# Optimization experiments

Hardware: AMD Instinct MI355X
Metric: run time of the kernel (lower is better)

Reference implementation:

```python
import jax, jax.numpy as jnp
import numpy as np

B, T, D = 1, 2048, 4096
N, K, H = 32, 8, 128  # num_heads, num_kv_heads, head_dim
ROPE_BASE = 10000
SCALE_FACTOR = 1.0
EPS = 1e-6
NEG_INF = -1e9


def rms_norm(x):
    var = jnp.mean(jnp.square(x), axis=-1, keepdims=True)
    return x * jax.lax.rsqrt(var + EPS)


def apply_rope(x, positions, base_frequency, scale_factor=1.0):
    # x: [B, L, num_heads, H], positions: [B, L]
    head_dim = x.shape[-1]
    fraction = 2.0 * jnp.arange(head_dim // 2, dtype=jnp.float32) / head_dim
    timescale = base_frequency ** fraction  # [H/2]
    sinusoid = positions[..., None].astype(jnp.float32) / timescale  # [B,L,H/2]
    sinusoid = sinusoid[..., None, :] / scale_factor  # [B,L,1,H/2]
    sin, cos = jnp.sin(sinusoid), jnp.cos(sinusoid)
    x1, x2 = jnp.split(x, 2, axis=-1)
    return jnp.concatenate([x1 * cos - x2 * sin, x2 * cos + x1 * sin], axis=-1)


def setup_inputs() -> dict:
    key = jax.random.key(0)
    ks = jax.random.split(key, 7)
    x = jax.random.normal(ks[0], (B, T, D), dtype=jnp.float32)
    segment_pos = jnp.broadcast_to(jnp.arange(T, dtype=jnp.int32)[None, :], (B, T))
    causal = jnp.tril(jnp.ones((T, T), dtype=bool))
    attn_mask = jnp.where(causal, 0.0, NEG_INF).astype(jnp.float32)[None]  # [B,T,S]
    attn_mask = jnp.broadcast_to(attn_mask, (B, T, T))
    q_w = jax.random.normal(ks[1], (N, D, H), dtype=jnp.float32) * (D ** -0.5)
    kv_w = jax.random.normal(ks[2], (2, K, D, H), dtype=jnp.float32) * (D ** -0.5)
    o_w = jax.random.normal(ks[3], (N, H, D), dtype=jnp.float32) * ((N * H) ** -0.5)
    q_scale = jax.random.normal(ks[4], (H,), dtype=jnp.float32) * 0.02  # RMSNorm scale (zeros-init style)
    k_scale = jax.random.normal(ks[5], (H,), dtype=jnp.float32) * 0.02
    return {"x": x, "segment_pos": segment_pos, "attn_mask": attn_mask,
            "q_w": q_w, "kv_w": kv_w, "o_w": o_w,
            "q_scale": q_scale, "k_scale": k_scale}


def reference(x, segment_pos, attn_mask, q_w, kv_w, o_w, q_scale, k_scale):
    # Projections
    q = jnp.einsum('BTD,NDH->BTNH', x, q_w)          # [B,T,N,H]
    kv = jnp.einsum('BSD,CKDH->CBSKH', x, kv_w)      # [2,B,S,K,H]
    k, v = kv[0], kv[1]
    # QK RMSNorm (with scale, (1+scale) convention) and value RMSNorm (no scale)
    q = rms_norm(q) * (1.0 + q_scale)
    k = rms_norm(k) * (1.0 + k_scale)
    v = rms_norm(v)
    # RoPE (standard path: positions are [B,L])
    q = apply_rope(q, segment_pos, ROPE_BASE, SCALE_FACTOR)
    k = apply_rope(k, segment_pos, ROPE_BASE, SCALE_FACTOR)
    # GQA grouping: [B,T,K,G,H]
    G = N // K
    qg = q.reshape(B, T, K, G, H)
    attn_logits = jnp.einsum('btkgh,bskh->bkgts', qg, k)  # [B,K,G,T,S]
    attn_logits = attn_logits + attn_mask[:, None, None, :, :]
    attn_weights = jax.nn.softmax(attn_logits, axis=-1).astype(v.dtype)
    out = jnp.einsum('bkgts,bskh->btkgh', attn_weights, v)  # [B,T,K,G,H]
    out = out.reshape(B, T, N, H)
    return jnp.einsum('BTNH,NHD->BTD', out, o_w)
```

## Files before the change

kernel.cpp:

```cpp
#include <hip/hip_runtime.h>
#include <stdint.h>


typedef __bf16 bf16x8 __attribute__((ext_vector_type(8)));
typedef float  f32x4  __attribute__((ext_vector_type(4)));

__device__ __forceinline__ uint16_t f2bf(float f) {
    union { float f; uint32_t u; } v; v.f = f;
    uint32_t r = v.u + 0x7fffu + ((v.u >> 16) & 1u);
    return (uint16_t)(r >> 16);
}

__device__ __forceinline__ void gload_lds16(const void* g, void* l) {
    __builtin_amdgcn_global_load_lds(
        (const __attribute__((address_space(1))) uint32_t*)g,
        (__attribute__((address_space(3))) uint32_t*)l, 16, 0, 0);
}

__global__ __launch_bounds__(256) void k_cvt_x(const float* __restrict__ x,
                                               uint16_t* __restrict__ xb) {
    int i = (blockIdx.x * 256 + threadIdx.x) * 8;
    int r = i >> 12, k = i & 4095;
    float4 a = *(const float4*)(x + i);
    float4 b = *(const float4*)(x + i + 4);
    uint16_t tmp[8];
    tmp[0] = f2bf(a.x); tmp[1] = f2bf(a.y); tmp[2] = f2bf(a.z); tmp[3] = f2bf(a.w);
    tmp[4] = f2bf(b.x); tmp[5] = f2bf(b.y); tmp[6] = f2bf(b.z); tmp[7] = f2bf(b.w);
    int dst = r * 4096 + (k & ~63) + (((((k >> 3) & 7) ^ (r & 7))) << 3);
    *(uint4*)(xb + dst) = *(uint4*)tmp;
}

__global__ __launch_bounds__(256) void k_prep_wt(const float* __restrict__ qw,
                                                 const float* __restrict__ kvw,
                                                 uint16_t* __restrict__ Wt) {
    const int hx = blockIdx.x, dx = blockIdx.y, m = blockIdx.z;
    const float* src = (m < 32) ? (qw + (size_t)m * 524288)
                                : (kvw + (size_t)(m - 32) * 524288);
    __shared__ uint16_t tile[64][65];
    const int t = threadIdx.x, d0 = dx * 64, h0 = hx * 64;
#pragma unroll
    for (int i = 0; i < 16; ++i) {
        int idx = i * 256 + t, r = idx >> 6, c = idx & 63;
        tile[r][c] = f2bf(src[(size_t)(d0 + r) * 128 + h0 + c]);
    }
    __syncthreads();
#pragma unroll
    for (int it = 0; it < 2; ++it) {
        int slot = it * 256 + t, hr = slot >> 3, cl = slot & 7;
        int R = m * 128 + h0 + hr;
        uint16_t tmp[8];
#pragma unroll
        for (int e = 0; e < 8; ++e) tmp[e] = tile[cl * 8 + e][hr];
        *(uint4*)&Wt[(size_t)R * 4096 + d0 + ((cl ^ (R & 7)) << 3)] = *(uint4*)tmp;
    }
}

__global__ __launch_bounds__(256) void k_prep_ot(const float* __restrict__ ow,
                                                 uint16_t* __restrict__ Ot) {
    const int dx = blockIdx.x, hx = blockIdx.y, n = blockIdx.z;
    const float* src = ow + (size_t)n * 524288;
    __shared__ uint16_t tile[64][65];
    const int t = threadIdx.x, h0 = hx * 64, d0 = dx * 64;
#pragma unroll
    for (int i = 0; i < 16; ++i) {
        int idx = i * 256 + t, r = idx >> 6, c = idx & 63;
        tile[r][c] = f2bf(src[(size_t)(h0 + r) * 4096 + d0 + c]);
    }
    __syncthreads();
#pragma unroll
    for (int it = 0; it < 2; ++it) {
        int slot = it * 256 + t, dr = slot >> 3, cl = slot & 7;
        int R = d0 + dr;
        uint16_t tmp[8];
#pragma unroll
        for (int e = 0; e < 8; ++e) tmp[e] = tile[cl * 8 + e][dr];
        *(uint4*)&Ot[(size_t)R * 4096 + n * 128 + h0 + ((cl ^ (R & 7)) << 3)] = *(uint4*)tmp;
    }
}


#define PH_BAR do { asm volatile("" ::: "memory"); \
                    __builtin_amdgcn_s_barrier(); \
                    asm volatile("" ::: "memory"); } while (0)
#define WAIT_LGKM do { asm volatile("s_waitcnt lgkmcnt(0)" ::: "memory"); \
                       __builtin_amdgcn_sched_barrier(0); } while (0)
#define WAIT_VM(N) do { asm volatile("s_waitcnt vmcnt(" #N ")" ::: "memory"); \
                        __builtin_amdgcn_sched_barrier(0); } while (0)

__global__ __launch_bounds__(512, 2) void k_gemm_qkv(const uint16_t* __restrict__ A,
                                                     const uint16_t* __restrict__ Bt,
                                                     const int* __restrict__ pos,
                                                     const float* __restrict__ qs,
                                                     const float* __restrict__ ks,
                                                     uint16_t* __restrict__ Qg,
                                                     uint16_t* __restrict__ Kg,
                                                     uint16_t* __restrict__ Vg) {
    extern __shared__ __align__(16) char smem[];
    uint16_t* lds = (uint16_t*)smem;
    const int Kd = 4096;
    const int t = threadIdx.x, wid = t >> 6, lane = t & 63;
    const int l16 = lane & 15, quad = lane >> 4;
    const int wr = wid >> 2, wc = wid & 3;
    const int bx = blockIdx.x, bm0 = blockIdx.y * 256, bn0 = bx * 256;

    f32x4 acc[8][4];
    const f32x4 z4 = {0.f, 0.f, 0.f, 0.f};
#pragma unroll
    for (int i = 0; i < 8; ++i)
#pragma unroll
        for (int j = 0; j < 4; ++j) acc[i][j] = z4;

    const int r0 = wid * 16 + (lane >> 2), c4 = lane & 3;
    const int sw2 = (r0 >> 1) & 3, sw7 = r0 & 7;
    const int offK0 = (((c4 ^ sw2)) ^ sw7) * 8;
    const int offK1 = ((4 + (c4 ^ sw2)) ^ sw7) * 8;
    const uint16_t* pA0 = A + (size_t)(bm0 + r0) * Kd;
    const uint16_t* pA1 = pA0 + (size_t)128 * Kd;
    const uint16_t* pB0 = Bt + (size_t)(bn0 + r0) * Kd;
    const uint16_t* pB1 = pB0 + (size_t)128 * Kd;
    uint16_t* stA = lds + wid * 512;
    uint16_t* stB = lds + 32768 + wid * 512;

    const int sA = (l16 >> 1) & 3;
    const int rdA = (wr * 128 + l16) * 32 + ((quad ^ sA) << 3);
    const int rdB = 32768 + (wc * 64 + l16) * 32 + ((quad ^ sA) << 3);

    bf16x8 af[8], bf0, bf1;

#define STAGE_A(SLAB, OFF, TT) do { \
    gload_lds16(pA0 + (size_t)(TT) * 64 + (OFF), stA + (SLAB) * 8192); \
    gload_lds16(pA1 + (size_t)(TT) * 64 + (OFF), stA + (SLAB) * 8192 + 4096); } while (0)
#define STAGE_B(SLAB, OFF, TT) do { \
    gload_lds16(pB0 + (size_t)(TT) * 64 + (OFF), stB + (SLAB) * 8192); \
    gload_lds16(pB1 + (size_t)(TT) * 64 + (OFF), stB + (SLAB) * 8192 + 4096); } while (0)
#define LOAD_AF(SLAB) do { _Pragma("unroll") \
    for (int i_ = 0; i_ < 8; ++i_) \
        af[i_] = *(const bf16x8*)&lds[(SLAB) * 8192 + rdA + i_ * 512]; } while (0)
#define LOAD_BF(SLAB, CH) do { \
    bf0 = *(const bf16x8*)&lds[(SLAB) * 8192 + rdB + (CH) * 1024]; \
    bf1 = *(const bf16x8*)&lds[(SLAB) * 8192 + rdB + (CH) * 1024 + 512]; } while (0)
#define MFMA_PH(CH) do { __builtin_amdgcn_s_setprio(1); \
    _Pragma("unroll") for (int i_ = 0; i_ < 8; ++i_) { \
        acc[i_][2*(CH)]   = __builtin_amdgcn_mfma_f32_16x16x32_bf16(af[i_], bf0, acc[i_][2*(CH)],   0, 0, 0); \
        acc[i_][2*(CH)+1] = __builtin_amdgcn_mfma_f32_16x16x32_bf16(af[i_], bf1, acc[i_][2*(CH)+1], 0, 0, 0); } \
    __builtin_amdgcn_s_setprio(0); } while (0)

#define TILE(TT, BUF) do { \
     \
    LOAD_AF(2*(BUF)); LOAD_BF(2*(BUF), 0); \
    STAGE_A((((BUF)^1)*2+1), offK1, (TT)+1); \
    PH_BAR; WAIT_LGKM; MFMA_PH(0); PH_BAR; \
     \
    LOAD_BF(2*(BUF), 1); \
    WAIT_VM(6); \
    STAGE_B((((BUF)^1)*2+1), offK1, (TT)+1); \
    PH_BAR; WAIT_LGKM; MFMA_PH(1); PH_BAR; \
     \
    LOAD_AF(2*(BUF)+1); LOAD_BF(2*(BUF)+1, 0); \
    STAGE_A((BUF)*2, offK0, (TT)+2); \
    PH_BAR; WAIT_LGKM; MFMA_PH(0); PH_BAR; \
     \
    LOAD_BF(2*(BUF)+1, 1); \
    WAIT_VM(6); \
    STAGE_B((BUF)*2, offK0, (TT)+2); \
    PH_BAR; WAIT_LGKM; MFMA_PH(1); PH_BAR; \
} while (0)

    STAGE_A(0, offK0, 0); STAGE_B(0, offK0, 0);
    STAGE_A(1, offK1, 0); STAGE_B(1, offK1, 0);
    STAGE_A(2, offK0, 1); STAGE_B(2, offK0, 1);
    WAIT_VM(8);
    PH_BAR;

#pragma unroll 1
    for (int Ti = 0; Ti < 31; ++Ti) {
        TILE(2 * Ti, 0);
        TILE(2 * Ti + 1, 1);
    }

    STAGE_A(3, offK1, 63); STAGE_B(3, offK1, 63);
    WAIT_VM(0);
    PH_BAR;
#pragma unroll
    for (int T = 62; T < 64; ++T) {
        const int BUF = T & 1;
        LOAD_AF(2*BUF);   LOAD_BF(2*BUF, 0);   PH_BAR; WAIT_LGKM; MFMA_PH(0); PH_BAR;
        LOAD_BF(2*BUF, 1);                     PH_BAR; WAIT_LGKM; MFMA_PH(1); PH_BAR;
        LOAD_AF(2*BUF+1); LOAD_BF(2*BUF+1, 0); PH_BAR; WAIT_LGKM; MFMA_PH(0); PH_BAR;
        LOAD_BF(2*BUF+1, 1);                   PH_BAR; WAIT_LGKM; MFMA_PH(1); PH_BAR;
    }

#undef TILE
#undef MFMA_PH
#undef LOAD_BF
#undef LOAD_AF
#undef STAGE_B
#undef STAGE_A

    float* X   = (float*)smem;
    float* ssq = (float*)(smem + 133120);

#pragma unroll
    for (int i = 0; i < 8; ++i)
#pragma unroll
        for (int r = 0; r < 4; ++r) {
            float s = 0.f;
#pragma unroll
            for (int j = 0; j < 4; ++j) s += acc[i][j][r] * acc[i][j][r];
            s += __shfl_xor(s, 1); s += __shfl_xor(s, 2);
            s += __shfl_xor(s, 4); s += __shfl_xor(s, 8);
            if (l16 == 0)
                ssq[(wr * 128 + i * 16 + quad * 4 + r) * 4 + (wc >> 1) * 2 + (wc & 1)] = s;
        }
    __syncthreads();

    const int cat = (bx < 16) ? 0 : (bx < 20 ? 1 : 2);
    float s1 = 0.f, s2 = 0.f, invts = 0.f;
    if (cat < 2) {
        const float* sc = cat ? ks : qs;
        s1 = 1.0f + sc[lane];
        s2 = 1.0f + sc[lane + 64];
        invts = exp2f((float)lane * -0.20762050593046014f);
    }

#pragma unroll
    for (int pass = 0; pass < 2; ++pass) {
        if (wr == pass) {
#pragma unroll
            for (int i = 0; i < 8; ++i)
#pragma unroll
                for (int j = 0; j < 4; ++j)
#pragma unroll
                    for (int r = 0; r < 4; ++r)
                        X[(i * 16 + quad * 4 + r) * 260 + wc * 64 + j * 16 + l16] = acc[i][j][r];
        }
        __syncthreads();
        for (int rr = 0; rr < 16; ++rr) {
            const int lrow = wid * 16 + rr;
            const int grow = bm0 + pass * 128 + lrow;
            float sn = 0.f, cs = 0.f;
            if (cat < 2) {
                float ang = (float)pos[grow] * invts;
                __sincosf(ang, &sn, &cs);
            }
#pragma unroll
            for (int hh = 0; hh < 2; ++hh) {
                const int sb = (pass * 128 + lrow) * 4 + hh * 2;
                float rn = rsqrtf((ssq[sb] + ssq[sb + 1]) * 0.0078125f + 1e-6f);
                float x1 = X[lrow * 260 + hh * 128 + lane];
                float x2 = X[lrow * 260 + hh * 128 + 64 + lane];
                if (cat < 2) {
                    float y1 = x1 * rn * s1, y2 = x2 * rn * s2;
                    X[lrow * 260 + hh * 128 + lane]      = y1 * cs - y2 * sn;
                    X[lrow * 260 + hh * 128 + 64 + lane] = y2 * cs + y1 * sn;
                } else {
                    X[lrow * 260 + hh * 128 + lane]      = x1 * rn;
                    X[lrow * 260 + hh * 128 + 64 + lane] = x2 * rn;
                }
            }
        }
        __syncthreads();
        if (cat == 2) {
#pragma unroll
            for (int it = 0; it < 8; ++it) {
                int slot = it * 512 + t, hh = slot >> 11, rem = slot & 2047;
                int h = rem >> 4, sc2 = rem & 15;
                uint16_t tmp[8];
#pragma unroll
                for (int e = 0; e < 8; ++e)
                    tmp[e] = f2bf(X[(sc2 * 8 + e) * 260 + hh * 128 + h]);
                int n = bx * 2 + hh;
                *(uint4*)&Vg[((size_t)(n - 40) * 128 + h) * 2048 + (bm0 + pass * 128)
                             + ((sc2 ^ (h & 15)) << 3)] = *(uint4*)tmp;
            }
        } else {
#pragma unroll
            for (int it = 0; it < 8; ++it) {
                int slot = it * 512 + t, hh = slot >> 11, rem = slot & 2047;
                int lrow = rem >> 4, c = rem & 15;
                int tg = bm0 + pass * 128 + lrow, n = bx * 2 + hh;
                f32x4 a = *(f32x4*)&X[lrow * 260 + hh * 128 + c * 8];
                f32x4 b = *(f32x4*)&X[lrow * 260 + hh * 128 + c * 8 + 4];
                uint16_t tmp[8];
#pragma unroll
                for (int e = 0; e < 4; ++e) { tmp[e] = f2bf(a[e]); tmp[4 + e] = f2bf(b[e]); }
                if (cat == 0)
                    *(uint4*)&Qg[((size_t)n * 2048 + tg) * 128 + c * 8] = *(uint4*)tmp;
                else
                    *(uint4*)&Kg[((size_t)(n - 32) * 2048 + tg) * 128
                                 + ((c ^ (tg & 15)) << 3)] = *(uint4*)tmp;
            }
        }
        __syncthreads();
    }
}

__global__ __launch_bounds__(256) void k_gemm2(const uint16_t* __restrict__ A,
                                               const uint16_t* __restrict__ Bt,
                                               float* __restrict__ C0,
                                               float* __restrict__ C1p,
                                               int M, int N, int Kd) {
    __shared__ uint16_t As[128 * 64];
    __shared__ uint16_t Bs[128 * 64];
    const int t = threadIdx.x;
    const int wave = t >> 6, lane = t & 63, l16 = lane & 15, quad = lane >> 4;
    const int wr = wave >> 1, wc = wave & 1;
    const int bm0 = blockIdx.y * 128, bn0 = blockIdx.x * 128;
    const int kz = blockIdx.z;
    const int sw = l16 & 7;
    float* C = kz ? C1p : C0;

    f32x4 acc[4][4];
    const f32x4 z4 = {0.f, 0.f, 0.f, 0.f};
#pragma unroll
    for (int i = 0; i < 4; ++i)
#pragma unroll
        for (int j = 0; j < 4; ++j) acc[i][j] = z4;

    const size_t laneOff = (size_t)(lane >> 3) * Kd + (lane & 7) * 8;
    const uint16_t* aBase = A  + (size_t)(bm0 + wave * 32) * Kd + laneOff;
    const uint16_t* bBase = Bt + (size_t)(bn0 + wave * 32) * Kd + laneOff;

    const int kbeg = kz * (Kd >> 1), kend = kbeg + (Kd >> 1);
    for (int kb = kbeg; kb < kend; kb += 64) {
        __syncthreads();
#pragma unroll
        for (int j = 0; j < 4; ++j) {
            gload_lds16(aBase + (size_t)j * 8 * Kd + kb, &As[(wave * 32 + j * 8) * 64]);
            gload_lds16(bBase + (size_t)j * 8 * Kd + kb, &Bs[(wave * 32 + j * 8) * 64]);
        }
        __syncthreads();
#pragma unroll
        for (int kc = 0; kc < 2; ++kc) {
            bf16x8 af[4], bf[4];
#pragma unroll
            for (int i = 0; i < 4; ++i)
                af[i] = *(const bf16x8*)&As[(wr * 64 + i * 16 + l16) * 64 + (((kc * 4 + quad) ^ sw) << 3)];
#pragma unroll
            for (int j = 0; j < 4; ++j)
                bf[j] = *(const bf16x8*)&Bs[(wc * 64 + j * 16 + l16) * 64 + (((kc * 4 + quad) ^ sw) << 3)];
#pragma unroll
            for (int i = 0; i < 4; ++i)
#pragma unroll
                for (int j = 0; j < 4; ++j)
                    acc[i][j] = __builtin_amdgcn_mfma_f32_16x16x32_bf16(af[i], bf[j], acc[i][j], 0, 0, 0);
        }
    }
#pragma unroll
    for (int i = 0; i < 4; ++i)
#pragma unroll
        for (int j = 0; j < 4; ++j) {
            int row = bm0 + wr * 64 + i * 16 + quad * 4;
            int col = bn0 + wc * 64 + j * 16 + l16;
            float* cp = C + (size_t)row * N + col;
            cp[0]             = acc[i][j][0];
            cp[(size_t)N]     = acc[i][j][1];
            cp[2 * (size_t)N] = acc[i][j][2];
            cp[3 * (size_t)N] = acc[i][j][3];
        }
}

__global__ __launch_bounds__(256) void k_reduce(float* __restrict__ out,
                                                const float* __restrict__ p) {
    int i = (blockIdx.x * 256 + threadIdx.x) * 4;
    float4 a = *(float4*)(out + i);
    float4 b = *(const float4*)(p + i);
    a.x += b.x; a.y += b.y; a.z += b.z; a.w += b.w;
    *(float4*)(out + i) = a;
}

__global__ __launch_bounds__(256) void k_attn(const uint16_t* __restrict__ Q,
                                              const uint16_t* __restrict__ K,
                                              const uint16_t* __restrict__ Vt,
                                              uint16_t* __restrict__ att) {
    __shared__ uint16_t sK[128 * 128];
    __shared__ uint16_t sV[128 * 128];
    const int p = blockIdx.x, n = blockIdx.y, kk = n >> 2;
    const int t = threadIdx.x, wave = t >> 6, lane = t & 63;
    const int l16 = lane & 15, quad = lane >> 4;
    const f32x4 z4 = {0.f, 0.f, 0.f, 0.f};

    const uint16_t* Kbase = K  + ((size_t)kk * 2048 + wave * 32 + (lane >> 4)) * 128 + (lane & 15) * 8;
    const uint16_t* Vbase = Vt + ((size_t)kk * 128  + wave * 32 + (lane >> 4)) * 2048 + (lane & 15) * 8;

    for (int half = 0; half < 2; ++half) {
        const int qt = half ? (31 - p) : p;
        const int q0 = qt * 64;
        const int nk = (qt >> 1) + 1;

        bf16x8 qf[4];
#pragma unroll
        for (int kc = 0; kc < 4; ++kc)
            qf[kc] = *(const bf16x8*)(Q + (size_t)(n * 2048 + q0 + wave * 16 + l16) * 128 + kc * 32 + quad * 8);

        f32x4 O[8];
#pragma unroll
        for (int h = 0; h < 8; ++h) O[h] = z4;
        float mrow[4], lrow[4];
#pragma unroll
        for (int r = 0; r < 4; ++r) { mrow[r] = -INFINITY; lrow[r] = 0.f; }

        for (int st = 0; st < nk; ++st) {
            const int s0 = st * 128;
            __syncthreads();
#pragma unroll
            for (int j = 0; j < 8; ++j) {
                gload_lds16(Kbase + (size_t)(s0 + j * 4) * 128, &sK[(wave * 32 + j * 4) * 128]);
                gload_lds16(Vbase + (size_t)j * 4 * 2048 + s0,  &sV[(wave * 32 + j * 4) * 128]);
            }
            __syncthreads();

            f32x4 S[8];
#pragma unroll
            for (int jn = 0; jn < 8; ++jn) S[jn] = z4;
#pragma unroll
            for (int jn = 0; jn < 8; ++jn) {
                int krow = jn * 16 + l16;
#pragma unroll
                for (int kc = 0; kc < 4; ++kc) {
                    bf16x8 b = *(const bf16x8*)&sK[krow * 128 + (((kc * 4 + quad) ^ l16) << 3)];
                    S[jn] = __builtin_amdgcn_mfma_f32_16x16x32_bf16(qf[kc], b, S[jn], 0, 0, 0);
                }
            }
            if (st == nk - 1) {
#pragma unroll
                for (int jn = 0; jn < 8; ++jn) {
                    int sc = s0 + jn * 16 + l16;
#pragma unroll
                    for (int r = 0; r < 4; ++r) {
                        int mr = q0 + wave * 16 + quad * 4 + r;
                        if (sc > mr) S[jn][r] = -INFINITY;
                    }
                }
            }
            float alpha[4];
#pragma unroll
            for (int r = 0; r < 4; ++r) {
                float mx = S[0][r];
#pragma unroll
                for (int jn = 1; jn < 8; ++jn) mx = fmaxf(mx, S[jn][r]);
                mx = fmaxf(mx, __shfl_xor(mx, 1));
                mx = fmaxf(mx, __shfl_xor(mx, 2));
                mx = fmaxf(mx, __shfl_xor(mx, 4));
                mx = fmaxf(mx, __shfl_xor(mx, 8));
                float mnew = fmaxf(mrow[r], mx);
                float a = __expf(mrow[r] - mnew);
                mrow[r] = mnew;
                float sum = 0.f;
#pragma unroll
                for (int jn = 0; jn < 8; ++jn) {
                    float e = __expf(S[jn][r] - mnew);
                    S[jn][r] = e;
                    sum += e;
                }
                sum += __shfl_xor(sum, 1);
                sum += __shfl_xor(sum, 2);
                sum += __shfl_xor(sum, 4);
                sum += __shfl_xor(sum, 8);
                lrow[r] = lrow[r] * a + sum;
                alpha[r] = a;
            }
#pragma unroll
            for (int h = 0; h < 8; ++h)
#pragma unroll
                for (int r = 0; r < 4; ++r) O[h][r] *= alpha[r];

            __syncthreads();
#pragma unroll
            for (int jn = 0; jn < 8; ++jn)
#pragma unroll
                for (int r = 0; r < 4; ++r) {
                    int prow = wave * 16 + quad * 4 + r;
                    int pcol = jn * 16 + l16;
                    sK[prow * 128 + ((pcol & 7) | ((((pcol >> 3) ^ prow) & 15) << 3))]
                        = f2bf(S[jn][r]);
                }
            bf16x8 pf[4];
#pragma unroll
            for (int ksv = 0; ksv < 4; ++ksv)
                pf[ksv] = *(const bf16x8*)&sK[(wave * 16 + l16) * 128 + (((ksv * 4 + quad) ^ l16) << 3)];
#pragma unroll
            for (int hj = 0; hj < 8; ++hj) {
                int vrow = hj * 16 + l16;
#pragma unroll
                for (int ksv = 0; ksv < 4; ++ksv) {
                    bf16x8 b = *(const bf16x8*)&sV[vrow * 128 + (((ksv * 4 + quad) ^ l16) << 3)];
                    O[hj] = __builtin_amdgcn_mfma_f32_16x16x32_bf16(pf[ksv], b, O[hj], 0, 0, 0);
                }
            }
        }

        __syncthreads();
        uint16_t* sO = &sK[wave * 2112];
        float inv[4];
#pragma unroll
        for (int r = 0; r < 4; ++r) inv[r] = 1.0f / lrow[r];
#pragma unroll
        for (int hj = 0; hj < 8; ++hj)
#pragma unroll
            for (int r = 0; r < 4; ++r)
                sO[(quad * 4 + r) * 132 + hj * 16 + l16] = f2bf(O[hj][r] * inv[r]);
#pragma unroll
        for (int it = 0; it < 4; ++it) {
            int slot = it * 64 + lane, rloc = slot >> 4, cl = slot & 15;
            bf16x8 v = *(const bf16x8*)&sO[rloc * 132 + cl * 8];
            int R = q0 + wave * 16 + rloc;
            size_t dst = (size_t)R * 4096 + n * 128 + ((cl & 8) << 3) + (((cl & 7) ^ (R & 7)) << 3);
            *(uint4*)&att[dst] = *(uint4*)&v;
        }
    }
}

extern "C" void kernel_launch(void* const* d_in, const int* in_sizes, int n_in,
                              void* d_out, int out_size, void* d_ws, size_t ws_size,
                              hipStream_t stream) {
    const float* x   = (const float*)d_in[0];
    const int*   sp  = (const int*)d_in[1];
    const float* qw  = (const float*)d_in[3];
    const float* kvw = (const float*)d_in[4];
    const float* ow  = (const float*)d_in[5];
    const float* qsc = (const float*)d_in[6];
    const float* ksc = (const float*)d_in[7];
    float* out = (float*)d_out;

    char* ws = (char*)d_ws;
    uint16_t* xb   = (uint16_t*)(ws);
    uint16_t* Wt   = (uint16_t*)(ws + (size_t)(16u << 20));
    uint16_t* Qb   = (uint16_t*)(ws + (size_t)(64u << 20));
    uint16_t* Kb   = (uint16_t*)(ws + (size_t)(80u << 20));
    uint16_t* Vtb  = (uint16_t*)(ws + (size_t)(84u << 20));
    uint16_t* att  = (uint16_t*)(ws);
    uint16_t* Ot   = (uint16_t*)(ws + (size_t)(16u << 20));
    float*    part = (float*)   (ws + (size_t)(48u << 20));

    static bool attr_done = false;
    if (!attr_done) {
        hipFuncSetAttribute(reinterpret_cast<const void*>(k_gemm_qkv),
                            hipFuncAttributeMaxDynamicSharedMemorySize, 137216);
        attr_done = true;
    }

    k_cvt_x    <<<4096, 256, 0, stream>>>(x, xb);
    k_prep_wt  <<<dim3(2, 64, 48), 256, 0, stream>>>(qw, kvw, Wt);
    k_gemm_qkv <<<dim3(24, 8), 512, 137216, stream>>>(xb, Wt, sp, qsc, ksc, Qb, Kb, Vtb);
    k_prep_ot  <<<dim3(64, 2, 32), 256, 0, stream>>>(ow, Ot);
    k_attn     <<<dim3(16, 32), 256, 0, stream>>>(Qb, Kb, Vtb, att);
    k_gemm2    <<<dim3(32, 16, 2), 256, 0, stream>>>(att, Ot, out, part, 2048, 4096, 4096);
    k_reduce   <<<8192, 256, 0, stream>>>(out, part);
}
```

Before: 553.3 us.

## Replace split-K output GEMM with pipelined 256x128 kernel and reorder QKV MFMA phases

The output projection drops split-K plus a separate reduce kernel and uses a new 512-thread kernel. It has 256x128 tiles, a 6-slab LDS ring fed by global_load_lds, and barrier-phased MFMA with priority hints. This removes the partial-sum write, the reduce pass and the single-buffered load/compute serialization of the old kernel. The QKV GEMM inner phase also changes from 8x2 fragments per phase to a 4x4 fragment grid, which reuses B fragments more per LDS read. The new kernel needs about 144KB of dynamic LDS and launches only 256 blocks, which may limit occupancy.

Result: faster. 530.6 us (-4.1%).

```diff
diff --git a/kernel.cpp b/kernel.cpp
--- a/kernel.cpp
+++ b/kernel.cpp
@@ -77,7 +77,6 @@
         *(uint4*)&Ot[(size_t)R * 4096 + n * 128 + h0 + ((cl ^ (R & 7)) << 3)] = *(uint4*)tmp;
     }
 }
-
 
 #define PH_BAR do { asm volatile("" ::: "memory"); \
                     __builtin_amdgcn_s_barrier(); \
@@ -125,7 +124,7 @@
     const int rdA = (wr * 128 + l16) * 32 + ((quad ^ sA) << 3);
     const int rdB = 32768 + (wc * 64 + l16) * 32 + ((quad ^ sA) << 3);
 
-    bf16x8 af[8], bf0, bf1;
+    bf16x8 af[4], bf[4];
 
 #define STAGE_A(SLAB, OFF, TT) do { \
     gload_lds16(pA0 + (size_t)(TT) * 64 + (OFF), stA + (SLAB) * 8192); \
@@ -133,37 +132,37 @@
 #define STAGE_B(SLAB, OFF, TT) do { \
     gload_lds16(pB0 + (size_t)(TT) * 64 + (OFF), stB + (SLAB) * 8192); \
     gload_lds16(pB1 + (size_t)(TT) * 64 + (OFF), stB + (SLAB) * 8192 + 4096); } while (0)
-#define LOAD_AF(SLAB) do { _Pragma("unroll") \
-    for (int i_ = 0; i_ < 8; ++i_) \
-        af[i_] = *(const bf16x8*)&lds[(SLAB) * 8192 + rdA + i_ * 512]; } while (0)
-#define LOAD_BF(SLAB, CH) do { \
-    bf0 = *(const bf16x8*)&lds[(SLAB) * 8192 + rdB + (CH) * 1024]; \
-    bf1 = *(const bf16x8*)&lds[(SLAB) * 8192 + rdB + (CH) * 1024 + 512]; } while (0)
-#define MFMA_PH(CH) do { __builtin_amdgcn_s_setprio(1); \
-    _Pragma("unroll") for (int i_ = 0; i_ < 8; ++i_) { \
-        acc[i_][2*(CH)]   = __builtin_amdgcn_mfma_f32_16x16x32_bf16(af[i_], bf0, acc[i_][2*(CH)],   0, 0, 0); \
-        acc[i_][2*(CH)+1] = __builtin_amdgcn_mfma_f32_16x16x32_bf16(af[i_], bf1, acc[i_][2*(CH)+1], 0, 0, 0); } \
+#define LOAD_AF4(SLAB, I0) do { _Pragma("unroll") \
+    for (int i_ = 0; i_ < 4; ++i_) \
+        af[i_] = *(const bf16x8*)&lds[(SLAB) * 8192 + rdA + ((I0) + i_) * 512]; } while (0)
+#define LOAD_BF4(SLAB) do { _Pragma("unroll") \
+    for (int j_ = 0; j_ < 4; ++j_) \
+        bf[j_] = *(const bf16x8*)&lds[(SLAB) * 8192 + rdB + j_ * 512]; } while (0)
+#define MFMA_PH(I0) do { __builtin_amdgcn_s_setprio(1); \
+    _Pragma("unroll") for (int i_ = 0; i_ < 4; ++i_) \
+        _Pragma("unroll") for (int j_ = 0; j_ < 4; ++j_) \
+            acc[(I0) + i_][j_] = __builtin_amdgcn_mfma_f32_16x16x32_bf16(af[i_], bf[j_], acc[(I0) + i_][j_], 0, 0, 0); \
     __builtin_amdgcn_s_setprio(0); } while (0)
 
 #define TILE(TT, BUF) do { \
      \
-    LOAD_AF(2*(BUF)); LOAD_BF(2*(BUF), 0); \
+    LOAD_BF4(2*(BUF)); LOAD_AF4(2*(BUF), 0); \
     STAGE_A((((BUF)^1)*2+1), offK1, (TT)+1); \
     PH_BAR; WAIT_LGKM; MFMA_PH(0); PH_BAR; \
      \
-    LOAD_BF(2*(BUF), 1); \
+    LOAD_AF4(2*(BUF), 4); \
     WAIT_VM(6); \
     STAGE_B((((BUF)^1)*2+1), offK1, (TT)+1); \
-    PH_BAR; WAIT_LGKM; MFMA_PH(1); PH_BAR; \
+    PH_BAR; WAIT_LGKM; MFMA_PH(4); PH_BAR; \
      \
-    LOAD_AF(2*(BUF)+1); LOAD_BF(2*(BUF)+1, 0); \
+    LOAD_BF4(2*(BUF)+1); LOAD_AF4(2*(BUF)+1, 0); \
     STAGE_A((BUF)*2, offK0, (TT)+2); \
     PH_BAR; WAIT_LGKM; MFMA_PH(0); PH_BAR; \
      \
-    LOAD_BF(2*(BUF)+1, 1); \
+    LOAD_AF4(2*(BUF)+1, 4); \
     WAIT_VM(6); \
     STAGE_B((BUF)*2, offK0, (TT)+2); \
-    PH_BAR; WAIT_LGKM; MFMA_PH(1); PH_BAR; \
+    PH_BAR; WAIT_LGKM; MFMA_PH(4); PH_BAR; \
 } while (0)
 
     STAGE_A(0, offK0, 0); STAGE_B(0, offK0, 0);
@@ -184,16 +183,16 @@
 #pragma unroll
     for (int T = 62; T < 64; ++T) {
         const int BUF = T & 1;
-        LOAD_AF(2*BUF);   LOAD_BF(2*BUF, 0);   PH_BAR; WAIT_LGKM; MFMA_PH(0); PH_BAR;
-        LOAD_BF(2*BUF, 1);                     PH_BAR; WAIT_LGKM; MFMA_PH(1); PH_BAR;
-        LOAD_AF(2*BUF+1); LOAD_BF(2*BUF+1, 0); PH_BAR; WAIT_LGKM; MFMA_PH(0); PH_BAR;
-        LOAD_BF(2*BUF+1, 1);                   PH_BAR; WAIT_LGKM; MFMA_PH(1); PH_BAR;
+        LOAD_BF4(2*BUF); LOAD_AF4(2*BUF, 0);     PH_BAR; WAIT_LGKM; MFMA_PH(0); PH_BAR;
+        LOAD_AF4(2*BUF, 4);                      PH_BAR; WAIT_LGKM; MFMA_PH(4); PH_BAR;
+        LOAD_BF4(2*BUF+1); LOAD_AF4(2*BUF+1, 0); PH_BAR; WAIT_LGKM; MFMA_PH(0); PH_BAR;
+        LOAD_AF4(2*BUF+1, 4);                    PH_BAR; WAIT_LGKM; MFMA_PH(4); PH_BAR;
     }
 
 #undef TILE
 #undef MFMA_PH
-#undef LOAD_BF
-#undef LOAD_AF
+#undef LOAD_BF4
+#undef LOAD_AF4
 #undef STAGE_B
 #undef STAGE_A
 
@@ -295,20 +294,16 @@
     }
 }
 
-__global__ __launch_bounds__(256) void k_gemm2(const uint16_t* __restrict__ A,
-                                               const uint16_t* __restrict__ Bt,
-                                               float* __restrict__ C0,
-                                               float* __restrict__ C1p,
-                                               int M, int N, int Kd) {
-    __shared__ uint16_t As[128 * 64];
-    __shared__ uint16_t Bs[128 * 64];
-    const int t = threadIdx.x;
-    const int wave = t >> 6, lane = t & 63, l16 = lane & 15, quad = lane >> 4;
-    const int wr = wave >> 1, wc = wave & 1;
-    const int bm0 = blockIdx.y * 128, bn0 = blockIdx.x * 128;
-    const int kz = blockIdx.z;
-    const int sw = l16 & 7;
-    float* C = kz ? C1p : C0;
+__global__ __launch_bounds__(512, 2) void k_gemm2p(const uint16_t* __restrict__ A,
+                                                   const uint16_t* __restrict__ Bt,
+                                                   float* __restrict__ C) {
+    extern __shared__ __align__(16) char smem2[];
+    uint16_t* lds = (uint16_t*)smem2;
+    const int Kd = 4096, Nn = 4096;
+    const int t = threadIdx.x, wid = t >> 6, lane = t & 63;
+    const int l16 = lane & 15, quad = lane >> 4;
+    const int wr = wid >> 1, wc = wid & 1;
+    const int bm0 = blockIdx.y * 256, bn0 = blockIdx.x * 128;
 
     f32x4 acc[4][4];
     const f32x4 z4 = {0.f, 0.f, 0.f, 0.f};
@@ -317,56 +312,85 @@
 #pragma unroll
         for (int j = 0; j < 4; ++j) acc[i][j] = z4;
 
-    const size_t laneOff = (size_t)(lane >> 3) * Kd + (lane & 7) * 8;
-    const uint16_t* aBase = A  + (size_t)(bm0 + wave * 32) * Kd + laneOff;
-    const uint16_t* bBase = Bt + (size_t)(bn0 + wave * 32) * Kd + laneOff;
-
-    const int kbeg = kz * (Kd >> 1), kend = kbeg + (Kd >> 1);
-    for (int kb = kbeg; kb < kend; kb += 64) {
-        __syncthreads();
-#pragma unroll
-        for (int j = 0; j < 4; ++j) {
-            gload_lds16(aBase + (size_t)j * 8 * Kd + kb, &As[(wave * 32 + j * 8) * 64]);
-            gload_lds16(bBase + (size_t)j * 8 * Kd + kb, &Bs[(wave * 32 + j * 8) * 64]);
-        }
-        __syncthreads();
-#pragma unroll
-        for (int kc = 0; kc < 2; ++kc) {
-            bf16x8 af[4], bf[4];
-#pragma unroll
-            for (int i = 0; i < 4; ++i)
-                af[i] = *(const bf16x8*)&As[(wr * 64 + i * 16 + l16) * 64 + (((kc * 4 + quad) ^ sw) << 3)];
-#pragma unroll
-            for (int j = 0; j < 4; ++j)
-                bf[j] = *(const bf16x8*)&Bs[(wc * 64 + j * 16 + l16) * 64 + (((kc * 4 + quad) ^ sw) << 3)];
-#pragma unroll
-            for (int i = 0; i < 4; ++i)
-#pragma unroll
-                for (int j = 0; j < 4; ++j)
-                    acc[i][j] = __builtin_amdgcn_mfma_f32_16x16x32_bf16(af[i], bf[j], acc[i][j], 0, 0, 0);
-        }
-    }
+    const int r0 = wid * 16 + (lane >> 2), c4 = lane & 3;
+    const int sw2 = (r0 >> 1) & 3, sw7 = r0 & 7;
+    const int offK0 = ((c4 ^ sw2) ^ sw7) * 8;
+    const int offK1 = ((4 + (c4 ^ sw2)) ^ sw7) * 8;
+    const uint16_t* pA0 = A + (size_t)(bm0 + r0) * Kd;
+    const uint16_t* pA1 = pA0 + (size_t)128 * Kd;
+    const uint16_t* pB0 = Bt + (size_t)(bn0 + r0) * Kd;
+    uint16_t* stA = lds + wid * 512;
+    uint16_t* stB = lds + 49152 + wid * 512;
+
+    const int sA = (l16 >> 1) & 3;
+    const int rdA = (wr * 64 + l16) * 32 + ((quad ^ sA) << 3);
+    const int rdB = 49152 + (wc * 64 + l16) * 32 + ((quad ^ sA) << 3);
+
+    bf16x8 af[4], bf[4];
+
+#define G2_STAGE(SLAB, OFF, TT) do { \
+    gload_lds16(pA0 + (size_t)(TT) * 64 + (OFF), stA + (SLAB) * 8192); \
+    gload_lds16(pA1 + (size_t)(TT) * 64 + (OFF), stA + (SLAB) * 8192 + 4096); \
+    gload_lds16(pB0 + (size_t)(TT) * 64 + (OFF), stB + (SLAB) * 4096); } while (0)
+
+#define G2_MFMA do { __builtin_amdgcn_s_setprio(1); \
+    _Pragma("unroll") for (int i_ = 0; i_ < 4; ++i_) \
+        _Pragma("unroll") for (int j_ = 0; j_ < 4; ++j_) \
+            acc[i_][j_] = __builtin_amdgcn_mfma_f32_16x16x32_bf16(af[i_], bf[j_], acc[i_][j_], 0, 0, 0); \
+    __builtin_amdgcn_s_setprio(0); } while (0)
+
+#define G2_LOAD(CS) do { _Pragma("unroll") \
+    for (int i_ = 0; i_ < 4; ++i_) \
+        af[i_] = *(const bf16x8*)&lds[(CS) * 8192 + rdA + i_ * 512]; \
+    _Pragma("unroll") for (int j_ = 0; j_ < 4; ++j_) \
+        bf[j_] = *(const bf16x8*)&lds[(CS) * 4096 + rdB + j_ * 512]; } while (0)
+
+#define G2_PH(CS, SG, OFF, TT) do { \
+    G2_LOAD(CS); \
+    WAIT_VM(6); \
+    G2_STAGE((SG), (OFF), (TT)); \
+    PH_BAR; WAIT_LGKM; G2_MFMA; PH_BAR; } while (0)
+
+#define G2_PHT(CS, VMN) do { \
+    G2_LOAD(CS); \
+    WAIT_VM(VMN); \
+    PH_BAR; WAIT_LGKM; G2_MFMA; PH_BAR; } while (0)
+
+    G2_STAGE(0, offK0, 0);
+    G2_STAGE(1, offK1, 0);
+    G2_STAGE(2, offK0, 1);
+    G2_STAGE(3, offK1, 1);
+    WAIT_VM(9);
+    PH_BAR;
+
+#pragma unroll 1
+    for (int Tb = 0; Tb < 60; Tb += 3) {
+        G2_PH(0, 4, offK0, Tb + 2);  G2_PH(1, 5, offK1, Tb + 2);
+        G2_PH(2, 0, offK0, Tb + 3);  G2_PH(3, 1, offK1, Tb + 3);
+        G2_PH(4, 2, offK0, Tb + 4);  G2_PH(5, 3, offK1, Tb + 4);
+    }
+    G2_PH(0, 4, offK0, 62);  G2_PH(1, 5, offK1, 62);
+    G2_PH(2, 0, offK0, 63);  G2_PH(3, 1, offK1, 63);
+    G2_PHT(4, 6); G2_PHT(5, 3); G2_PHT(0, 0); G2_PHT(1, 0);
+
+#undef G2_PHT
+#undef G2_PH
+#undef G2_LOAD
+#undef G2_MFMA
+#undef G2_STAGE
+
 #pragma unroll
     for (int i = 0; i < 4; ++i)
 #pragma unroll
         for (int j = 0; j < 4; ++j) {
             int row = bm0 + wr * 64 + i * 16 + quad * 4;
             int col = bn0 + wc * 64 + j * 16 + l16;
-            float* cp = C + (size_t)row * N + col;
-            cp[0]             = acc[i][j][0];
-            cp[(size_t)N]     = acc[i][j][1];
-            cp[2 * (size_t)N] = acc[i][j][2];
-            cp[3 * (size_t)N] = acc[i][j][3];
-        }
-}
-
-__global__ __launch_bounds__(256) void k_reduce(float* __restrict__ out,
-                                                const float* __restrict__ p) {
-    int i = (blockIdx.x * 256 + threadIdx.x) * 4;
-    float4 a = *(float4*)(out + i);
-    float4 b = *(const float4*)(p + i);
-    a.x += b.x; a.y += b.y; a.z += b.z; a.w += b.w;
-    *(float4*)(out + i) = a;
+            float* cp = C + (size_t)row * Nn + col;
+            cp[0]              = acc[i][j][0];
+            cp[(size_t)Nn]     = acc[i][j][1];
+            cp[2 * (size_t)Nn] = acc[i][j][2];
+            cp[3 * (size_t)Nn] = acc[i][j][3];
+        }
 }
 
 __global__ __launch_bounds__(256) void k_attn(const uint16_t* __restrict__ Q,
@@ -531,12 +555,13 @@
     uint16_t* Vtb  = (uint16_t*)(ws + (size_t)(84u << 20));
     uint16_t* att  = (uint16_t*)(ws);
     uint16_t* Ot   = (uint16_t*)(ws + (size_t)(16u << 20));
-    float*    part = (float*)   (ws + (size_t)(48u << 20));
 
     static bool attr_done = false;
     if (!attr_done) {
         hipFuncSetAttribute(reinterpret_cast<const void*>(k_gemm_qkv),
                             hipFuncAttributeMaxDynamicSharedMemorySize, 137216);
+        hipFuncSetAttribute(reinterpret_cast<const void*>(k_gemm2p),
+                            hipFuncAttributeMaxDynamicSharedMemorySize, 147456);
         attr_done = true;
     }
 
@@ -545,6 +570,5 @@
     k_gemm_qkv <<<dim3(24, 8), 512, 137216, stream>>>(xb, Wt, sp, qsc, ksc, Qb, Kb, Vtb);
     k_prep_ot  <<<dim3(64, 2, 32), 256, 0, stream>>>(ow, Ot);
     k_attn     <<<dim3(16, 32), 256, 0, stream>>>(Qb, Kb, Vtb, att);
-    k_gemm2    <<<dim3(32, 16, 2), 256, 0, stream>>>(att, Ot, out, part, 2048, 4096, 4096);
-    k_reduce   <<<8192, 256, 0, stream>>>(out, part);
-}
+    k_gemm2p   <<<dim3(32, 8), 512, 147456, stream>>>(att, Ot, out);
+}
```
